# Optimization experiments

Hardware: AMD Instinct MI355X
Metric: run time of the kernel (lower is better)

Reference implementation:

```python
import jax, jax.numpy as jnp
import numpy as np
from jax import lax

# dims
B, N, K = 8, 16384, 16          # clouds, points/cloud, neighbors per cluster
M1 = N // K
R0, R1 = 0.2, 0.5                # radii
D0, D1 = 128, 512                # local feature dim, global latent dim
H0, H1, HD0, HD1 = 64, 256, 256, 128


def setup_inputs() -> dict:
    key = jax.random.key(0)
    ks = jax.random.split(key, 20)
    def w(k, shape):
        return jax.random.normal(k, shape, jnp.float32) / np.sqrt(shape[0])
    points = jax.random.normal(ks[0], (B, N, 3), jnp.float32)
    return dict(
        points=points,
        # encoder 0: shared MLP on relative coords, max-pool over K
        W0a=w(ks[1], (3, H0)), b0a=jnp.zeros((H0,), jnp.float32),
        W0b=w(ks[2], (H0, D0)), b0b=jnp.zeros((D0,), jnp.float32),
        # encoder 1 (global): concat(rel coords, local feats) -> MLP -> global max
        W1a=w(ks[3], (3 + D0, H1)), b1a=jnp.zeros((H1,), jnp.float32),
        W1b=w(ks[4], (H1, D1)), b1b=jnp.zeros((D1,), jnp.float32),
        # decoder 0: latent + learned 2D grid -> rel points + child feats
        grid0=jax.random.normal(ks[5], (M1, 2), jnp.float32),
        Wd0a=w(ks[6], (D1 + 2, HD0)), bd0a=jnp.zeros((HD0,), jnp.float32),
        Wp0=w(ks[7], (HD0, 3)), Wf0=w(ks[8], (HD0, D0)),
        # decoder 1: per-point feat + learned 2D grid -> rel points (x16)
        grid1=jax.random.normal(ks[9], (K, 2), jnp.float32),
        Wd1a=w(ks[10], (D0 + 2, HD1)), bd1a=jnp.zeros((HD1,), jnp.float32),
        Wp1=w(ks[11], (HD1, 3)),
    )


def _fps(pts, m):
    """Farthest point sampling: m indices into pts [N,3]. Indices are non-diff."""
    p = lax.stop_gradient(pts)
    d = jnp.sum((p - p[0]) ** 2, axis=-1)          # dist to seed point 0
    def body(i, st):
        idxs, dists = st
        nxt = jnp.argmax(dists).astype(jnp.int32)
        idxs = idxs.at[i].set(nxt)
        dnew = jnp.sum((p - p[nxt]) ** 2, axis=-1)
        return idxs, jnp.minimum(dists, dnew)
    idxs = jnp.zeros((m,), jnp.int32)
    idxs, _ = lax.fori_loop(1, m, body, (idxs, d))
    return idxs


def reference(points, W0a, b0a, W0b, b0b, W1a, b1a, W1b, b1b,
              grid0, Wd0a, bd0a, Wp0, Wf0, grid1, Wd1a, bd1a, Wp1):
    def fwd_cloud(pts):  # pts [N,3]
        # ---- encode ----
        fidx = _fps(pts, M1)
        p1 = pts[fidx]                                               # [M1,3] anchors
        q = lax.stop_gradient(p1); s = lax.stop_gradient(pts)
        d2 = jnp.sum((q[:, None, :] - s[None, :, :]) ** 2, axis=-1)  # [M1,N]
        negd, knn = lax.top_k(-d2, K)                                # [M1,K]
        within = (-negd) <= R0 * R0                                  # radius mask
        neigh = pts[knn]                                             # [M1,K,3]
        rel0 = (neigh - p1[:, None, :]) / R0
        rel0 = jnp.where(within[:, :, None], rel0, 0.0)              # out-of-radius -> anchor
        h = jax.nn.relu(rel0 @ W0a + b0a) @ W0b + b0b                # [M1,K,D0]
        f0 = jnp.max(h, axis=1)                                      # [M1,D0] local feats
        rel1 = p1 / R1                                               # complete-encoding last layer
        h1 = jax.nn.relu(jnp.concatenate([rel1, f0], -1) @ W1a + b1a) @ W1b + b1b
        z = jnp.max(h1, axis=0)                                      # [D1] global latent
        # ---- decode ----
        zt = jnp.broadcast_to(z, (M1, D1))
        hd0 = jax.nn.relu(jnp.concatenate([zt, grid0], -1) @ Wd0a + bd0a)
        relp0 = hd0 @ Wp0                                            # [M1,3]
        fdec = hd0 @ Wf0                                             # [M1,D0]
        xt = jnp.concatenate([jnp.repeat(fdec[:, None, :], K, axis=1),
                              jnp.broadcast_to(grid1, (M1, K, 2))], -1)
        relp1 = (jax.nn.relu(xt @ Wd1a + bd1a) @ Wp1).reshape(M1 * K, 3)
        # construct_output_points (complete_encoding branch)
        out1 = relp0 * R1                                            # [M1,3]
        clus = jnp.repeat(jnp.arange(M1), K)                         # decoder clusters
        out0 = out1[clus] + relp1 * R0                               # [M1*K,3]
        # get_used_input_points
        ip1 = p1                                                     # level-1 inputs
        ip0 = pts[knn.reshape(-1)]                                   # [M1*K,3] level-0 inputs
        return ip0, ip1, out0, out1, z
    return jax.vmap(fwd_cloud)(points)
```

## Files before the change

kernel.cpp:

```cpp
#include <hip/hip_runtime.h>

#define NB 8
#define NPTS 16384
#define M1 1024
#define NA 8192

#define OUT_IP0  0
#define OUT_IP1  393216
#define OUT_OUT0 417792
#define OUT_OUT1 811008
#define OUT_Z    835584

typedef unsigned long long u64;

__device__ __forceinline__ float exact_d2(float ax, float ay, float az,
                                          float bx, float by, float bz) {
  float dx = __fsub_rn(ax, bx);
  float dy = __fsub_rn(ay, by);
  float dz = __fsub_rn(az, bz);
  return __fadd_rn(__fadd_rn(__fmul_rn(dx, dx), __fmul_rn(dy, dy)),
                   __fmul_rn(dz, dz));
}

__device__ __forceinline__ bool dl_lt(float d1, int i1, float d2, int i2) {
  return (d1 < d2) || ((d1 == d2) && (i1 < i2));
}

template <int CTRL>
__device__ __forceinline__ float dpp_fmax(float v) {
  const int s =
      __builtin_amdgcn_update_dpp(0, __float_as_int(v), CTRL, 0xf, 0xf, true);
  return fmaxf(v, __int_as_float(s));
}

template <int CTRL>
__device__ __forceinline__ float dpp_fmin_self(float v) {
  const int s = __builtin_amdgcn_update_dpp(__float_as_int(v),
                                            __float_as_int(v), CTRL, 0xf, 0xf,
                                            false);
  return fminf(v, __int_as_float(s));
}

template <int CTRL>
__device__ __forceinline__ u64 dpp_min_u64(u64 v) {
  const int lo = (int)(unsigned)v;
  const int hi = (int)(unsigned)(v >> 32);
  const int slo = __builtin_amdgcn_update_dpp(lo, lo, CTRL, 0xf, 0xf, false);
  const int shi = __builtin_amdgcn_update_dpp(hi, hi, CTRL, 0xf, 0xf, false);
  const u64 s = ((u64)(unsigned)shi << 32) | (unsigned)slo;
  return s < v ? s : v;
}

__global__ __launch_bounds__(1024) void fps_kernel(
    const float* __restrict__ pts, int* __restrict__ fidx) {
  const int b = blockIdx.x;
  const float* __restrict__ P = pts + (size_t)b * NPTS * 3;
  const int t = threadIdx.x;
  const int lane = t & 63;

  __shared__ u64 s_slot[3];
  __shared__ char s_pad[81920];
  if ((int)blockIdx.x == -1) ((volatile char*)s_pad)[0] = 1;

  float px[16], py[16], pz[16], dd[16];
  const float sx = P[0], sy = P[1], sz = P[2];
  const int base = t * 16;
  float bv = -1.0f;
  int bj = 0;
#pragma unroll
  for (int j = 0; j < 16; ++j) {
    const float x = P[(base + j) * 3 + 0];
    const float y = P[(base + j) * 3 + 1];
    const float z = P[(base + j) * 3 + 2];
    px[j] = x; py[j] = y; pz[j] = z;
    const float d = exact_d2(x, y, z, sx, sy, sz);
    dd[j] = d;
    if (d > bv) { bv = d; bj = j; }
  }
  if (t == 0) {
    fidx[b * M1 + 0] = 0;
    s_slot[0] = 0; s_slot[1] = 0; s_slot[2] = 0;
  }
  __syncthreads();

  for (int it = 1; it < M1; ++it) {
    const int par = it % 3;
    const int nxt = (it + 1) % 3;
    float wm = bv;
    wm = dpp_fmax<0x111>(wm);
    wm = dpp_fmax<0x112>(wm);
    wm = dpp_fmax<0x114>(wm);
    wm = dpp_fmax<0x118>(wm);
    wm = dpp_fmax<0x142>(wm);
    wm = dpp_fmax<0x143>(wm);
    wm = __int_as_float(
        __builtin_amdgcn_readlane(__float_as_int(wm), 63));
    const unsigned long long msk = __ballot(bv == wm);
    const int l0 = (int)__ffsll((long long)msk) - 1;
    const int wbi = __builtin_amdgcn_readlane(base + bj, l0);
    if (lane == 0) {
      const u64 key =
          ((u64)__float_as_uint(wm) << 32) | (u64)(~(unsigned)wbi);
      atomicMax(&s_slot[par], key);
    }
    if (t == 0) s_slot[nxt] = 0;
    __syncthreads();
    const u64 g = s_slot[par];
    const int wi = __builtin_amdgcn_readfirstlane((int)(~(unsigned)g));
    if (t == 0) fidx[b * M1 + it] = wi;
    const float cx = P[wi * 3 + 0];
    const float cy = P[wi * 3 + 1];
    const float cz = P[wi * 3 + 2];
    bv = -1.0f; bj = 0;
#pragma unroll
    for (int j = 0; j < 16; ++j) {
      const float d2 = exact_d2(px[j], py[j], pz[j], cx, cy, cz);
      const float nd = fminf(dd[j], d2);
      dd[j] = nd;
      if (nd > bv) { bv = nd; bj = j; }
    }
  }
}

__global__ void gather_p1_kernel(const float* __restrict__ pts,
                                 const int* __restrict__ fidx,
                                 float* __restrict__ p1,
                                 float* __restrict__ out_ip1) {
  const int i = blockIdx.x * 256 + threadIdx.x;
  if (i >= NA * 3) return;
  const int a = i / 3, c = i - a * 3;
  const int b = a >> 10;
  const int src = fidx[a];
  const float v = pts[((size_t)b * NPTS + src) * 3 + c];
  p1[i] = v;
  out_ip1[i] = v;
}

__global__ __launch_bounds__(256) void knn_kernel(
    const float* __restrict__ pts, const float* __restrict__ p1,
    int* __restrict__ knn_i, float* __restrict__ knn_d,
    float* __restrict__ out_ip0) {
  const int wq = threadIdx.x >> 6;
  const int lane = threadIdx.x & 63;
  const int a = blockIdx.x * 4 + wq;
  const int b = a >> 10;
  const float* __restrict__ P = pts + (size_t)b * NPTS * 3;
  const float qx = p1[a * 3 + 0], qy = p1[a * 3 + 1], qz = p1[a * 3 + 2];
  const float INF = __builtin_inff();
  float D[16]; int I[16];
#pragma unroll
  for (int s = 0; s < 16; ++s) { D[s] = INF; I[s] = 0x7fffffff; }
  float wstar = INF;

  for (int s = 0; s < NPTS / 64; ++s) {
    const int idx = s * 64 + lane;
    const float x = P[idx * 3 + 0];
    const float y = P[idx * 3 + 1];
    const float z = P[idx * 3 + 2];
    const float d2 = exact_d2(x, y, z, qx, qy, qz);
    const bool pass = (d2 <= wstar);
    if (__any(pass)) {
      if (pass && dl_lt(d2, idx, D[15], I[15])) {
        bool c[16];
#pragma unroll
        for (int u = 0; u < 16; ++u) c[u] = dl_lt(d2, idx, D[u], I[u]);
#pragma unroll
        for (int u = 15; u >= 1; --u) {
          D[u] = c[u] ? (c[u - 1] ? D[u - 1] : d2) : D[u];
          I[u] = c[u] ? (c[u - 1] ? I[u - 1] : idx) : I[u];
        }
        if (c[0]) { D[0] = d2; I[0] = idx; }
      }
      float w = D[15];
      w = dpp_fmin_self<0x111>(w);
      w = dpp_fmin_self<0x112>(w);
      w = dpp_fmin_self<0x114>(w);
      w = dpp_fmin_self<0x118>(w);
      w = dpp_fmin_self<0x142>(w);
      w = dpp_fmin_self<0x143>(w);
      wstar = __int_as_float(
          __builtin_amdgcn_readlane(__float_as_int(w), 63));
    }
  }

  __shared__ u64 sk[4][1024];
#pragma unroll
  for (int u = 0; u < 16; ++u)
    sk[wq][lane * 16 + u] =
        ((u64)__float_as_uint(D[u]) << 32) | (unsigned)I[u];
  int head = lane * 16;
  const int hend = head + 16;
  u64 md = sk[wq][head];
  u64 outK = 0;
  for (int r = 0; r < 16; ++r) {
    u64 v = md;
    v = dpp_min_u64<0x111>(v);
    v = dpp_min_u64<0x112>(v);
    v = dpp_min_u64<0x114>(v);
    v = dpp_min_u64<0x118>(v);
    v = dpp_min_u64<0x142>(v);
    v = dpp_min_u64<0x143>(v);
    const unsigned glo =
        (unsigned)__builtin_amdgcn_readlane((int)(unsigned)v, 63);
    const unsigned ghi =
        (unsigned)__builtin_amdgcn_readlane((int)(unsigned)(v >> 32), 63);
    const u64 g = ((u64)ghi << 32) | glo;
    if (lane == r) outK = g;
    if (md == g) {
      ++head;
      md = (head < hend) ? sk[wq][head] : ~0ull;
    }
  }
  if (lane < 16) {
    const int o = a * 16 + lane;
    const int outI = (int)(unsigned)outK;
    knn_i[o] = outI;
    knn_d[o] = __uint_as_float((unsigned)(outK >> 32));
    out_ip0[(size_t)o * 3 + 0] = P[outI * 3 + 0];
    out_ip0[(size_t)o * 3 + 1] = P[outI * 3 + 1];
    out_ip0[(size_t)o * 3 + 2] = P[outI * 3 + 2];
  }
}

__global__ __launch_bounds__(128) void enc0_kernel(
    const float* __restrict__ ip0, const float* __restrict__ knn_d,
    const float* __restrict__ p1, const float* __restrict__ W0a,
    const float* __restrict__ b0a, const float* __restrict__ W0b,
    const float* __restrict__ b0b, float* __restrict__ f0) {
  const int a = blockIdx.x;
  __shared__ float rel[16][4];
  __shared__ __align__(16) float h1s[16][64];
  const int t = threadIdx.x;
  if (t < 16) {
    const float ax = p1[a * 3 + 0], ay = p1[a * 3 + 1], az = p1[a * 3 + 2];
    const float kd = knn_d[a * 16 + t];
    const bool within = (kd <= 0.04f);
    const float* nb = ip0 + (size_t)(a * 16 + t) * 3;
    rel[t][0] = within ? (nb[0] - ax) * 5.0f : 0.0f;
    rel[t][1] = within ? (nb[1] - ay) * 5.0f : 0.0f;
    rel[t][2] = within ? (nb[2] - az) * 5.0f : 0.0f;
  }
  __syncthreads();
  {
    const int m = t & 63, kh = t >> 6;
    const float w0 = W0a[m], w1 = W0a[64 + m], w2 = W0a[128 + m];
    const float bb = b0a[m];
#pragma unroll
    for (int kk = 0; kk < 8; ++kk) {
      const int k = kh * 8 + kk;
      const float h =
          fmaf(rel[k][0], w0, fmaf(rel[k][1], w1, fmaf(rel[k][2], w2, bb)));
      h1s[k][m] = fmaxf(h, 0.0f);
    }
  }
  __syncthreads();
  {
    const int col = t;
    float acc[16];
#pragma unroll
    for (int k = 0; k < 16; ++k) acc[k] = 0.0f;
    for (int m = 0; m < 64; m += 4) {
      const float w0 = W0b[(m + 0) * 128 + col];
      const float w1 = W0b[(m + 1) * 128 + col];
      const float w2 = W0b[(m + 2) * 128 + col];
      const float w3 = W0b[(m + 3) * 128 + col];
#pragma unroll
      for (int k = 0; k < 16; ++k) {
        const float4 h = *(const float4*)&h1s[k][m];
        acc[k] = fmaf(h.x, w0, fmaf(h.y, w1, fmaf(h.z, w2, fmaf(h.w, w3, acc[k]))));
      }
    }
    float mx = acc[0];
#pragma unroll
    for (int k = 1; k < 16; ++k) mx = fmaxf(mx, acc[k]);
    f0[(size_t)a * 128 + col] = mx + b0b[col];
  }
}

__global__ void build_x1_kernel(const float* __restrict__ p1,
                                const float* __restrict__ f0,
                                float* __restrict__ X1) {
  const int i = blockIdx.x * 256 + threadIdx.x;
  if (i >= NA * 132) return;
  const int r = i / 132, c = i - r * 132;
  float v;
  if (c < 3) v = p1[r * 3 + c] * 2.0f;
  else if (c < 131) v = f0[(size_t)r * 128 + (c - 3)];
  else v = 0.0f;
  X1[i] = v;
}

template <int DO_RELU, int COLMAX>
__global__ __launch_bounds__(256) void gemm64_kernel(
    const float* __restrict__ A, const float* __restrict__ W,
    const float* __restrict__ bias, float* __restrict__ C, const int N,
    const int K, const int Kreal, const int lda, const int ldb) {
  __shared__ float As[64][33];
  __shared__ __align__(16) float Bs[32][64];
  __shared__ float red[16][64];
  const int t = threadIdx.x;
  const int tx = t & 15, ty = t >> 4;
  const int row0 = blockIdx.y * 64, col0 = blockIdx.x * 64;
  float acc[4][4] = {};
  for (int k0 = 0; k0 < K; k0 += 32) {
    {
      const int m = t >> 2, kk = (t & 3) * 8;
      const float* src = A + (size_t)(row0 + m) * lda + (k0 + kk);
#pragma unroll
      for (int u = 0; u < 8; ++u)
        As[m][kk + u] = (k0 + kk + u < Kreal) ? src[u] : 0.0f;
    }
    {
      const int kk = t >> 3, c = (t & 7) * 8;
      const int kg = k0 + kk;
      const float* src = W + (size_t)kg * ldb + (col0 + c);
      const bool ok = (kg < Kreal);
#pragma unroll
      for (int u = 0; u < 8; ++u) Bs[kk][c + u] = ok ? src[u] : 0.0f;
    }
    __syncthreads();
#pragma unroll
    for (int k = 0; k < 32; ++k) {
      const float a0 = As[ty * 4 + 0][k];
      const float a1 = As[ty * 4 + 1][k];
      const float a2 = As[ty * 4 + 2][k];
      const float a3 = As[ty * 4 + 3][k];
      const float4 bv = *(const float4*)&Bs[k][tx * 4];
      acc[0][0] = fmaf(a0, bv.x, acc[0][0]);
      acc[0][1] = fmaf(a0, bv.y, acc[0][1]);
      acc[0][2] = fmaf(a0, bv.z, acc[0][2]);
      acc[0][3] = fmaf(a0, bv.w, acc[0][3]);
      acc[1][0] = fmaf(a1, bv.x, acc[1][0]);
      acc[1][1] = fmaf(a1, bv.y, acc[1][1]);
      acc[1][2] = fmaf(a1, bv.z, acc[1][2]);
      acc[1][3] = fmaf(a1, bv.w, acc[1][3]);
      acc[2][0] = fmaf(a2, bv.x, acc[2][0]);
      acc[2][1] = fmaf(a2, bv.y, acc[2][1]);
      acc[2][2] = fmaf(a2, bv.z, acc[2][2]);
      acc[2][3] = fmaf(a2, bv.w, acc[2][3]);
      acc[3][0] = fmaf(a3, bv.x, acc[3][0]);
      acc[3][1] = fmaf(a3, bv.y, acc[3][1]);
      acc[3][2] = fmaf(a3, bv.z, acc[3][2]);
      acc[3][3] = fmaf(a3, bv.w, acc[3][3]);
    }
    __syncthreads();
  }
  const float b0v = bias[col0 + tx * 4 + 0];
  const float b1v = bias[col0 + tx * 4 + 1];
  const float b2v = bias[col0 + tx * 4 + 2];
  const float b3v = bias[col0 + tx * 4 + 3];
  if (COLMAX == 0) {
#pragma unroll
    for (int i = 0; i < 4; ++i) {
      float4 v;
      v.x = acc[i][0] + b0v;
      v.y = acc[i][1] + b1v;
      v.z = acc[i][2] + b2v;
      v.w = acc[i][3] + b3v;
      if (DO_RELU) {
        v.x = fmaxf(v.x, 0.0f); v.y = fmaxf(v.y, 0.0f);
        v.z = fmaxf(v.z, 0.0f); v.w = fmaxf(v.w, 0.0f);
      }
      *(float4*)&C[(size_t)(row0 + ty * 4 + i) * N + col0 + tx * 4] = v;
    }
  } else {
    const float m0 =
        fmaxf(fmaxf(acc[0][0], acc[1][0]), fmaxf(acc[2][0], acc[3][0])) + b0v;
    const float m1 =
        fmaxf(fmaxf(acc[0][1], acc[1][1]), fmaxf(acc[2][1], acc[3][1])) + b1v;
    const float m2 =
        fmaxf(fmaxf(acc[0][2], acc[1][2]), fmaxf(acc[2][2], acc[3][2])) + b2v;
    const float m3 =
        fmaxf(fmaxf(acc[0][3], acc[1][3]), fmaxf(acc[2][3], acc[3][3])) + b3v;
    red[ty][tx * 4 + 0] = m0;
    red[ty][tx * 4 + 1] = m1;
    red[ty][tx * 4 + 2] = m2;
    red[ty][tx * 4 + 3] = m3;
    __syncthreads();
    if (t < 64) {
      float mm = red[0][t];
#pragma unroll
      for (int r = 1; r < 16; ++r) mm = fmaxf(mm, red[r][t]);
      C[(size_t)(row0 >> 6) * N + col0 + t] = mm;
    }
  }
}

__global__ __launch_bounds__(1024) void zwfused_kernel(
    const float* __restrict__ pmax, const float* __restrict__ Wd0a,
    float* __restrict__ outz, float* __restrict__ zW) {
  const int b = blockIdx.x;
  const int t = threadIdx.x;
  __shared__ float zs[512];
  __shared__ float part[4][256];
  if (t < 512) {
    float m = pmax[(size_t)(b * 16) * 512 + t];
#pragma unroll
    for (int rt = 1; rt < 16; ++rt)
      m = fmaxf(m, pmax[(size_t)(b * 16 + rt) * 512 + t]);
    zs[t] = m;
    outz[b * 512 + t] = m;
  }
  __syncthreads();
  const int c = t & 255;
  const int ch = t >> 8;
  const int q0 = ch * 128;
  float acc = 0.0f;
  for (int q = 0; q < 128; q += 4) {
    acc = fmaf(zs[q0 + q + 0], Wd0a[(q0 + q + 0) * 256 + c], acc);
    acc = fmaf(zs[q0 + q + 1], Wd0a[(q0 + q + 1) * 256 + c], acc);
    acc = fmaf(zs[q0 + q + 2], Wd0a[(q0 + q + 2) * 256 + c], acc);
    acc = fmaf(zs[q0 + q + 3], Wd0a[(q0 + q + 3) * 256 + c], acc);
  }
  part[ch][c] = acc;
  __syncthreads();
  if (t < 256)
    zW[b * 256 + t] =
        (part[0][t] + part[1][t]) + (part[2][t] + part[3][t]);
}

__global__ __launch_bounds__(256) void dec0_kernel(
    const float* __restrict__ zW, const float* __restrict__ grid0,
    const float* __restrict__ Wd0a, const float* __restrict__ bd0a,
    const float* __restrict__ Wf0, const float* __restrict__ Wp0,
    float* __restrict__ fdec, float* __restrict__ out_out1) {
  const int blk = blockIdx.x;
  const int b = blk >> 5;
  const int m0 = (blk & 31) * 32;
  __shared__ __align__(16) float hd0s[32][256];
  __shared__ float g0s[32][2];
  __shared__ float wp0s[768];
  const int t = threadIdx.x;
  if (t < 64) {
    const int r = t >> 1, cc = t & 1;
    g0s[r][cc] = grid0[(m0 + r) * 2 + cc];
  }
  wp0s[t] = Wp0[t];
  wp0s[256 + t] = Wp0[256 + t];
  wp0s[512 + t] = Wp0[512 + t];
  __syncthreads();
  {
    const int c = t;
    const float w0 = Wd0a[512 * 256 + c];
    const float w1 = Wd0a[513 * 256 + c];
    const float basev = zW[b * 256 + c] + bd0a[c];
#pragma unroll 8
    for (int r = 0; r < 32; ++r) {
      const float h = fmaf(g0s[r][0], w0, fmaf(g0s[r][1], w1, basev));
      hd0s[r][c] = fmaxf(h, 0.0f);
    }
  }
  __syncthreads();
  {
    const int c = t & 127;
    const int rh = (t >> 7) * 16;
    float acc[16];
#pragma unroll
    for (int r = 0; r < 16; ++r) acc[r] = 0.0f;
    for (int q = 0; q < 256; q += 4) {
      const float w0 = Wf0[(q + 0) * 128 + c];
      const float w1 = Wf0[(q + 1) * 128 + c];
      const float w2 = Wf0[(q + 2) * 128 + c];
      const float w3 = Wf0[(q + 3) * 128 + c];
#pragma unroll
      for (int r = 0; r < 16; ++r) {
        const float4 h = *(const float4*)&hd0s[rh + r][q];
        acc[r] = fmaf(h.x, w0, fmaf(h.y, w1, fmaf(h.z, w2, fmaf(h.w, w3, acc[r]))));
      }
    }
    const size_t g0i = ((size_t)(b * M1 + m0 + rh)) * 128 + c;
#pragma unroll
    for (int r = 0; r < 16; ++r) fdec[g0i + (size_t)r * 128] = acc[r];
  }
  if (t < 96) {
    const int m = t / 3;
    const int c = t - m * 3;
    float acc = 0.0f;
    for (int q = 0; q < 256; ++q) acc = fmaf(hd0s[m][q], wp0s[q * 3 + c], acc);
    out_out1[((size_t)(b * M1 + m0 + m)) * 3 + c] = acc * 0.5f;
  }
}

__global__ __launch_bounds__(256) void dec1_kernel(
    const float* __restrict__ fdec, const float* __restrict__ grid1,
    const float* __restrict__ Wd1a, const float* __restrict__ bd1a,
    const float* __restrict__ Wp1, const float* __restrict__ out1r,
    float* __restrict__ out0w) {
  const int a0 = blockIdx.x * 16;
  __shared__ __align__(16) float fds[16][128];
  __shared__ __align__(16) float gs[16][128];
  __shared__ __align__(16) float us[16][128];
  __shared__ __align__(16) float wp1t[3][128];
  __shared__ float o1s[16][3];
  const int t = threadIdx.x;
  {
    const int r = t >> 4;
    const int c0 = (t & 15) * 8;
    const float* src = fdec + ((size_t)(a0 + r)) * 128 + c0;
#pragma unroll
    for (int u = 0; u < 8; ++u) fds[r][c0 + u] = src[u];
  }
  {
    const int k = t >> 4;
    const int c0 = (t & 15) * 8;
    const float g0 = grid1[k * 2 + 0];
    const float g1 = grid1[k * 2 + 1];
#pragma unroll
    for (int u = 0; u < 8; ++u) {
      const int c = c0 + u;
      gs[k][c] = fmaf(g0, Wd1a[128 * 128 + c], fmaf(g1, Wd1a[129 * 128 + c], bd1a[c]));
    }
  }
  if (t < 128) {
    wp1t[0][t] = Wp1[t * 3 + 0];
    wp1t[1][t] = Wp1[t * 3 + 1];
    wp1t[2][t] = Wp1[t * 3 + 2];
  }
  if (t < 48) {
    const int r = t / 3, c = t - r * 3;
    o1s[r][c] = out1r[((size_t)(a0 + r)) * 3 + c];
  }
  __syncthreads();
  {
    const int c = t & 127;
    const int mh = (t >> 7) * 8;
    float acc[8];
#pragma unroll
    for (int r = 0; r < 8; ++r) acc[r] = 0.0f;
    for (int q = 0; q < 128; q += 4) {
      const float w0 = Wd1a[(q + 0) * 128 + c];
      const float w1 = Wd1a[(q + 1) * 128 + c];
      const float w2 = Wd1a[(q + 2) * 128 + c];
      const float w3 = Wd1a[(q + 3) * 128 + c];
#pragma unroll
      for (int r = 0; r < 8; ++r) {
        const float4 f = *(const float4*)&fds[mh + r][q];
        acc[r] = fmaf(f.x, w0, fmaf(f.y, w1, fmaf(f.z, w2, fmaf(f.w, w3, acc[r]))));
      }
    }
#pragma unroll
    for (int r = 0; r < 8; ++r) us[mh + r][c] = acc[r];
  }
  __syncthreads();
  {
    const int m = t >> 4, k = t & 15;
    float a0v = 0.0f, a1v = 0.0f, a2v = 0.0f;
    for (int c = 0; c < 128; c += 4) {
      const float4 uu = *(const float4*)&us[m][c];
      const float4 gg = *(const float4*)&gs[k][c];
      const float h0 = fmaxf(uu.x + gg.x, 0.0f);
      const float h1 = fmaxf(uu.y + gg.y, 0.0f);
      const float h2 = fmaxf(uu.z + gg.z, 0.0f);
      const float h3 = fmaxf(uu.w + gg.w, 0.0f);
      const float4 wx = *(const float4*)&wp1t[0][c];
      const float4 wy = *(const float4*)&wp1t[1][c];
      const float4 wz = *(const float4*)&wp1t[2][c];
      a0v = fmaf(h0, wx.x, fmaf(h1, wx.y, fmaf(h2, wx.z, fmaf(h3, wx.w, a0v))));
      a1v = fmaf(h0, wy.x, fmaf(h1, wy.y, fmaf(h2, wy.z, fmaf(h3, wy.w, a1v))));
      a2v = fmaf(h0, wz.x, fmaf(h1, wz.y, fmaf(h2, wz.z, fmaf(h3, wz.w, a2v))));
    }
    const size_t o = (((size_t)(a0 + m)) * 16 + k) * 3;
    out0w[o + 0] = o1s[m][0] + a0v * 0.2f;
    out0w[o + 1] = o1s[m][1] + a1v * 0.2f;
    out0w[o + 2] = o1s[m][2] + a2v * 0.2f;
  }
}

extern "C" void kernel_launch(void* const* d_in, const int* in_sizes, int n_in,
                              void* d_out_v, int out_size, void* d_ws,
                              size_t ws_size, hipStream_t stream) {
  (void)in_sizes; (void)n_in; (void)out_size; (void)ws_size;
  const float* points = (const float*)d_in[0];
  const float* W0a = (const float*)d_in[1];
  const float* b0a = (const float*)d_in[2];
  const float* W0b = (const float*)d_in[3];
  const float* b0b = (const float*)d_in[4];
  const float* W1a = (const float*)d_in[5];
  const float* b1a = (const float*)d_in[6];
  const float* W1b = (const float*)d_in[7];
  const float* b1b = (const float*)d_in[8];
  const float* grid0 = (const float*)d_in[9];
  const float* Wd0a = (const float*)d_in[10];
  const float* bd0a = (const float*)d_in[11];
  const float* Wp0 = (const float*)d_in[12];
  const float* Wf0 = (const float*)d_in[13];
  const float* grid1 = (const float*)d_in[14];
  const float* Wd1a = (const float*)d_in[15];
  const float* bd1a = (const float*)d_in[16];
  const float* Wp1 = (const float*)d_in[17];
  float* out = (float*)d_out_v;
  char* ws = (char*)d_ws;

  int* fidx = (int*)(ws + 0);
  int* knn_i = (int*)(ws + 32768);
  float* knn_d = (float*)(ws + 557056);
  float* p1 = (float*)(ws + 1081344);
  float* f0 = (float*)(ws + 1179648);
  float* X1 = (float*)(ws + 5373952);
  float* mid1 = (float*)(ws + 9699328);
  float* pmax = (float*)(ws + 18087936);
  float* zW = (float*)(ws + 18366464);
  float* fdec = (float*)(ws + 18374656);

  fps_kernel<<<NB, 1024, 0, stream>>>(points, fidx);
  gather_p1_kernel<<<(NA * 3 + 255) / 256, 256, 0, stream>>>(points, fidx, p1,
                                                             out + OUT_IP1);
  knn_kernel<<<NA / 4, 256, 0, stream>>>(points, p1, knn_i, knn_d,
                                         out + OUT_IP0);
  enc0_kernel<<<NA, 128, 0, stream>>>(out + OUT_IP0, knn_d, p1, W0a, b0a, W0b,
                                      b0b, f0);
  build_x1_kernel<<<(NA * 132 + 255) / 256, 256, 0, stream>>>(p1, f0, X1);
  gemm64_kernel<1, 0><<<dim3(4, 128), 256, 0, stream>>>(X1, W1a, b1a, mid1,
                                                        256, 132, 131, 132, 256);
  gemm64_kernel<0, 1><<<dim3(8, 128), 256, 0, stream>>>(mid1, W1b, b1b, pmax,
                                                        512, 256, 256, 256, 512);
  zwfused_kernel<<<NB, 1024, 0, stream>>>(pmax, Wd0a, out + OUT_Z, zW);
  dec0_kernel<<<256, 256, 0, stream>>>(zW, grid0, Wd0a, bd0a, Wf0, Wp0, fdec,
                                       out + OUT_OUT1);
  dec1_kernel<<<NA / 16, 256, 0, stream>>>(fdec, grid1, Wd1a, bd1a, Wp1,
                                           out + OUT_OUT1, out + OUT_OUT0);
}
```

Before: 2.280 ms.

## Spatially sort points and skip FPS distance updates with bounding-sphere test

Adds a counting-sort kernel that buckets each cloud's points into a 16^3 grid, so each FPS thread owns 16 spatially nearby points. Each thread computes a bounding sphere over its points and skips the distance update when the new centre is provably farther than its current maximum. The reduction now carries a packed 64-bit (distance, inverted original index) key, which replaces the ballot/readlane index recovery and keeps first-index tie-breaking. In exchange it adds an extra kernel launch, gathered loads through the permutation, and a 64-bit DPP reduction with twice the lane shuffles. The skip only saves work when a whole wavefront skips, and it leaves the per-iteration barrier cost unchanged.

```diff
diff --git a/kernel.cpp b/kernel.cpp
--- a/kernel.cpp
+++ b/kernel.cpp
@@ -24,13 +24,6 @@
 
 __device__ __forceinline__ bool dl_lt(float d1, int i1, float d2, int i2) {
   return (d1 < d2) || ((d1 == d2) && (i1 < i2));
-}
-
-template <int CTRL>
-__device__ __forceinline__ float dpp_fmax(float v) {
-  const int s =
-      __builtin_amdgcn_update_dpp(0, __float_as_int(v), CTRL, 0xf, 0xf, true);
-  return fmaxf(v, __int_as_float(s));
 }
 
 template <int CTRL>
@@ -51,8 +44,66 @@
   return s < v ? s : v;
 }
 
+template <int CTRL>
+__device__ __forceinline__ u64 dpp_max_u64(u64 v) {
+  const int lo = (int)(unsigned)v;
+  const int hi = (int)(unsigned)(v >> 32);
+  const int slo = __builtin_amdgcn_update_dpp(lo, lo, CTRL, 0xf, 0xf, false);
+  const int shi = __builtin_amdgcn_update_dpp(hi, hi, CTRL, 0xf, 0xf, false);
+  const u64 s = ((u64)(unsigned)shi << 32) | (unsigned)slo;
+  return s > v ? s : v;
+}
+
+__global__ __launch_bounds__(1024) void sort_kernel(
+    const float* __restrict__ pts, int* __restrict__ perm) {
+  const int b = blockIdx.x;
+  const float* __restrict__ P = pts + (size_t)b * NPTS * 3;
+  const int t = threadIdx.x;
+  __shared__ int hist[4096];
+  __shared__ int csum[64];
+  for (int i = t; i < 4096; i += 1024) hist[i] = 0;
+  __syncthreads();
+  int cell[16];
+#pragma unroll
+  for (int j = 0; j < 16; ++j) {
+    const int idx = t * 16 + j;
+    const float x = P[idx * 3 + 0];
+    const float y = P[idx * 3 + 1];
+    const float z = P[idx * 3 + 2];
+    int cx = (int)((x + 4.0f) * 2.0f); cx = cx < 0 ? 0 : (cx > 15 ? 15 : cx);
+    int cy = (int)((y + 4.0f) * 2.0f); cy = cy < 0 ? 0 : (cy > 15 ? 15 : cy);
+    int cz = (int)((z + 4.0f) * 2.0f); cz = cz < 0 ? 0 : (cz > 15 ? 15 : cz);
+    const int c = (cx << 8) | (cy << 4) | cz;
+    cell[j] = c;
+    atomicAdd(&hist[c], 1);
+  }
+  __syncthreads();
+  if (t < 64) {
+    int s = 0;
+    for (int i = 0; i < 64; ++i) s += hist[t * 64 + i];
+    csum[t] = s;
+  }
+  __syncthreads();
+  if (t == 0) {
+    int run = 0;
+    for (int i = 0; i < 64; ++i) { const int v = csum[i]; csum[i] = run; run += v; }
+  }
+  __syncthreads();
+  if (t < 64) {
+    int run = csum[t];
+    for (int i = 0; i < 64; ++i) { const int v = hist[t * 64 + i]; hist[t * 64 + i] = run; run += v; }
+  }
+  __syncthreads();
+#pragma unroll
+  for (int j = 0; j < 16; ++j) {
+    const int pos = atomicAdd(&hist[cell[j]], 1);
+    perm[b * NPTS + pos] = t * 16 + j;
+  }
+}
+
 __global__ __launch_bounds__(1024) void fps_kernel(
-    const float* __restrict__ pts, int* __restrict__ fidx) {
+    const float* __restrict__ pts, const int* __restrict__ perm,
+    int* __restrict__ fidx) {
   const int b = blockIdx.x;
   const float* __restrict__ P = pts + (size_t)b * NPTS * 3;
   const int t = threadIdx.x;
@@ -63,20 +114,34 @@
   if ((int)blockIdx.x == -1) ((volatile char*)s_pad)[0] = 1;
 
   float px[16], py[16], pz[16], dd[16];
+  int oi[16];
   const float sx = P[0], sy = P[1], sz = P[2];
-  const int base = t * 16;
-  float bv = -1.0f;
-  int bj = 0;
+  u64 kb = 0;
+  float mx = 0.0f, my = 0.0f, mz = 0.0f;
 #pragma unroll
   for (int j = 0; j < 16; ++j) {
-    const float x = P[(base + j) * 3 + 0];
-    const float y = P[(base + j) * 3 + 1];
-    const float z = P[(base + j) * 3 + 2];
+    const int o = perm[b * NPTS + t * 16 + j];
+    oi[j] = o;
+    const float x = P[o * 3 + 0];
+    const float y = P[o * 3 + 1];
+    const float z = P[o * 3 + 2];
     px[j] = x; py[j] = y; pz[j] = z;
+    mx += x; my += y; mz += z;
     const float d = exact_d2(x, y, z, sx, sy, sz);
     dd[j] = d;
-    if (d > bv) { bv = d; bj = j; }
-  }
+    const u64 k = ((u64)__float_as_uint(d) << 32) | (u64)(~(unsigned)o);
+    if (k > kb) kb = k;
+  }
+  mx *= 0.0625f; my *= 0.0625f; mz *= 0.0625f;
+  float r2m = 0.0f;
+#pragma unroll
+  for (int j = 0; j < 16; ++j) {
+    const float dx = px[j] - mx, dy = py[j] - my, dz = pz[j] - mz;
+    const float r2 = fmaf(dx, dx, fmaf(dy, dy, dz * dz));
+    r2m = fmaxf(r2m, r2);
+  }
+  const float r = sqrtf(r2m) * 1.01f;
+
   if (t == 0) {
     fidx[b * M1 + 0] = 0;
     s_slot[0] = 0; s_slot[1] = 0; s_slot[2] = 0;
@@ -86,38 +151,44 @@
   for (int it = 1; it < M1; ++it) {
     const int par = it % 3;
     const int nxt = (it + 1) % 3;
-    float wm = bv;
-    wm = dpp_fmax<0x111>(wm);
-    wm = dpp_fmax<0x112>(wm);
-    wm = dpp_fmax<0x114>(wm);
-    wm = dpp_fmax<0x118>(wm);
-    wm = dpp_fmax<0x142>(wm);
-    wm = dpp_fmax<0x143>(wm);
-    wm = __int_as_float(
-        __builtin_amdgcn_readlane(__float_as_int(wm), 63));
-    const unsigned long long msk = __ballot(bv == wm);
-    const int l0 = (int)__ffsll((long long)msk) - 1;
-    const int wbi = __builtin_amdgcn_readlane(base + bj, l0);
-    if (lane == 0) {
-      const u64 key =
-          ((u64)__float_as_uint(wm) << 32) | (u64)(~(unsigned)wbi);
-      atomicMax(&s_slot[par], key);
-    }
+    u64 v = kb;
+    v = dpp_max_u64<0x111>(v);
+    v = dpp_max_u64<0x112>(v);
+    v = dpp_max_u64<0x114>(v);
+    v = dpp_max_u64<0x118>(v);
+    v = dpp_max_u64<0x142>(v);
+    v = dpp_max_u64<0x143>(v);
+    const unsigned wlo =
+        (unsigned)__builtin_amdgcn_readlane((int)(unsigned)v, 63);
+    const unsigned whi =
+        (unsigned)__builtin_amdgcn_readlane((int)(unsigned)(v >> 32), 63);
+    if (lane == 0) atomicMax(&s_slot[par], ((u64)whi << 32) | wlo);
     if (t == 0) s_slot[nxt] = 0;
     __syncthreads();
     const u64 g = s_slot[par];
-    const int wi = __builtin_amdgcn_readfirstlane((int)(~(unsigned)g));
+    const int wi =
+        __builtin_amdgcn_readfirstlane((int)(~(unsigned)g)) & (NPTS - 1);
     if (t == 0) fidx[b * M1 + it] = wi;
     const float cx = P[wi * 3 + 0];
     const float cy = P[wi * 3 + 1];
     const float cz = P[wi * 3 + 2];
-    bv = -1.0f; bj = 0;
-#pragma unroll
-    for (int j = 0; j < 16; ++j) {
-      const float d2 = exact_d2(px[j], py[j], pz[j], cx, cy, cz);
-      const float nd = fminf(dd[j], d2);
-      dd[j] = nd;
-      if (nd > bv) { bv = nd; bj = j; }
+    const float bvf = __uint_as_float((unsigned)(kb >> 32));
+    const float ex = mx - cx, ey = my - cy, ez = mz - cz;
+    const float d2mc = fmaf(ex, ex, fmaf(ey, ey, ez * ez));
+    const float s = sqrtf(d2mc);
+    const float lb = fmaf(s, 0.995f, -r);
+    const bool skip = (lb > 0.0f) && (lb * lb * 0.98f >= bvf);
+    if (!skip) {
+      kb = 0;
+#pragma unroll
+      for (int j = 0; j < 16; ++j) {
+        const float d2 = exact_d2(px[j], py[j], pz[j], cx, cy, cz);
+        const float nd = fminf(dd[j], d2);
+        dd[j] = nd;
+        const u64 k =
+            ((u64)__float_as_uint(nd) << 32) | (u64)(~(unsigned)oi[j]);
+        if (k > kb) kb = k;
+      }
     }
   }
 }
@@ -598,11 +669,13 @@
   float* f0 = (float*)(ws + 1179648);
   float* X1 = (float*)(ws + 5373952);
   float* mid1 = (float*)(ws + 9699328);
+  int* perm = (int*)(ws + 12000000);
   float* pmax = (float*)(ws + 18087936);
   float* zW = (float*)(ws + 18366464);
   float* fdec = (float*)(ws + 18374656);
 
-  fps_kernel<<<NB, 1024, 0, stream>>>(points, fidx);
+  sort_kernel<<<NB, 1024, 0, stream>>>(points, perm);
+  fps_kernel<<<NB, 1024, 0, stream>>>(points, perm, fidx);
   gather_p1_kernel<<<(NA * 3 + 255) / 256, 256, 0, stream>>>(points, fidx, p1,
                                                              out + OUT_IP1);
   knn_kernel<<<NA / 4, 256, 0, stream>>>(points, p1, knn_i, knn_d,
```

After: 3.043 ms, median of 2. +33.5%, slower.
